# Kernel tuning notes

Measured on AMD Instinct MI355X. Metric: run time of the kernel, lower is better.

## Reference

```python
import jax, jax.numpy as jnp
import numpy as np

N_HEAD = 8
EPS = 1e-6  # LayerNorm2d eps


def setup_inputs() -> dict:
    key = jax.random.key(0)
    ks = jax.random.split(key, 7)
    B, C, H, W = 16, 256, 128, 128
    nh, dk, dv = N_HEAD, 32, 32
    s = 1.0 / np.sqrt(C)
    return {
        "q": jax.random.normal(ks[0], (B, C, H, W), jnp.float32),
        "k": jax.random.normal(ks[1], (B, C, H, W), jnp.float32),
        "v": jax.random.normal(ks[2], (B, C, H, W), jnp.float32),
        # 1x1 convs without bias == channel matmuls; weight shape [out_ch, in_ch]
        "wq": jax.random.normal(ks[3], (nh * dk, C), jnp.float32) * s,
        "wk": jax.random.normal(ks[4], (nh * dk, C), jnp.float32) * s,
        "wv": jax.random.normal(ks[5], (nh * dv, C), jnp.float32) * s,
        "wfc": jax.random.normal(ks[6], (C, nh * dv), jnp.float32) * (1.0 / np.sqrt(nh * dv)),
        "ln_w": jnp.ones((C,), jnp.float32),
        "ln_b": jnp.zeros((C,), jnp.float32),
        "kernel": 5,
        "pad": 2,
    }


def _forward(q, k, v, wq, wk, wv, wfc, ln_w, ln_b, kernel, pad):
    B, C, H, W = q.shape
    nh = N_HEAD
    dk = wq.shape[0] // nh
    dv = wv.shape[0] // nh
    assert kernel == 2 * pad + 1
    residual = q
    # 1x1 conv projections, split into heads: [B, nh, d, H, W]
    qh = jnp.einsum('oc,bchw->bohw', wq, q).reshape(B, nh, dk, H, W)
    kh = jnp.einsum('oc,bchw->bohw', wk, k).reshape(B, nh, dk, H, W)
    vh = jnp.einsum('oc,bchw->bohw', wv, v).reshape(B, nh, dv, H, W)
    # zero-pad spatially: out-of-bounds correlations/values are zero, matching the
    # original bilinear sampler (zeros padding) and the custom padding() helper.
    kp = jnp.pad(kh, ((0, 0), (0, 0), (0, 0), (pad, pad), (pad, pad)))
    vp = jnp.pad(vh, ((0, 0), (0, 0), (0, 0), (pad, pad), (pad, pad)))
    # local correlation volume: dot(q[i,j], k[i+dy-pad, j+dx-pad]) for the KxK window
    # (integer offsets -> bilinear sample degenerates to a gather). Never materializes
    # the full [B, HW, HW] matrix the torch code builds before sampling.
    corr = jnp.stack(
        [jnp.einsum('bncij,bncij->bnij', qh, kp[:, :, :, dy:dy + H, dx:dx + W])
         for dy in range(kernel) for dx in range(kernel)], axis=-1)  # [B,nh,H,W,K*K]
    # relu (from CorrBlock.corr), temperature = sqrt(d_k), softmax over window.
    # OOB entries are 0 (not -inf), faithfully matching the original.
    attn = jax.nn.softmax(jax.nn.relu(corr) / jnp.float32(np.sqrt(dk)), axis=-1)
    # channel attention: per-pixel weighted sum of v over the same window
    out = jnp.zeros((B, nh, dv, H, W), q.dtype)
    idx = 0
    for dy in range(kernel):
        for dx in range(kernel):
            out = out + attn[:, :, :, :, idx][:, :, None] * vp[:, :, :, dy:dy + H, dx:dx + W]
            idx += 1
    o = jnp.einsum('oc,bchw->bohw', wfc, out.reshape(B, nh * dv, H, W)) + residual
    # LayerNorm2d: normalize over channel dim per pixel
    mu = o.mean(1, keepdims=True)
    var = ((o - mu) ** 2).mean(1, keepdims=True)
    y = (o - mu) / jnp.sqrt(var + EPS)
    return ln_w[None, :, None, None] * y + ln_b[None, :, None, None]


def reference(q, k, v, wq, wk, wv, wfc, ln_w, ln_b, kernel, pad):
    return _forward(q, k, v, wq, wk, wv, wfc, ln_w, ln_b, kernel, pad)
```

## Files before the change

### kernel.cpp

```cpp
#include <hip/hip_runtime.h>
#include <hip/hip_bf16.h>

#define BATCH 16
#define CH 256
#define HH 128
#define WW 128
#define HWSZ (HH * WW)
#define NHEAD 8
#define DHEAD 32
#define PW 132
#define PPIX (132 * 132)
#define ROWS 264
#define ASTR 40

typedef __attribute__((ext_vector_type(8))) short bf16x8;
typedef __attribute__((ext_vector_type(4))) float f32x4;
typedef _Float16 h2v __attribute__((ext_vector_type(2)));

__device__ __forceinline__ unsigned short f2h(float f) {
    _Float16 h = (_Float16)f;
    return __builtin_bit_cast(unsigned short, h);
}
__device__ __forceinline__ unsigned pkbf(float a, float b) {
    __hip_bfloat162_raw r = __hip_bfloat162_raw(__float22bfloat162_rn(make_float2(a, b)));
    return (unsigned)r.x | ((unsigned)r.y << 16);
}
__device__ __forceinline__ int swzc(int row, int chunk) { return chunk ^ ((row >> 2) & 7); }

#if __has_builtin(__builtin_amdgcn_fdot2)
#define DOT2(a, b, c) __builtin_amdgcn_fdot2((a), (b), (c), false)
#else
#define DOT2(a, b, c) ((c) + (float)(a)[0] * (float)(b)[0] + (float)(a)[1] * (float)(b)[1])
#endif

__global__ __launch_bounds__(256)
void zpad_kernel(unsigned short* __restrict__ kpad, unsigned short* __restrict__ vpad)
{
    int bid = blockIdx.x;
    unsigned short* dst = ((bid & 1) ? vpad : kpad) + (size_t)(bid >> 1) * PPIX * DHEAD;
    const uint4 z = {0u, 0u, 0u, 0u};
    for (int i = threadIdx.x; i < 1040; i += 256) {
        int row, col;
        if (i < 264)      { row = i / 132; col = i - row * 132; }
        else if (i < 528) { int j = i - 264; int r = j / 132; row = 130 + r; col = j - r * 132; }
        else              { int j = i - 528; row = 2 + (j >> 2); int c = j & 3; col = (c < 2) ? c : (128 + c); }
        uint4* p = reinterpret_cast<uint4*>(dst + (size_t)(row * PW + col) * DHEAD);
        p[0] = z; p[1] = z; p[2] = z; p[3] = z;
    }
}

__global__ __launch_bounds__(256)
void prep_kernel(const float* __restrict__ wq, const float* __restrict__ wk,
                 const float* __restrict__ wv, const float* __restrict__ wfc,
                 unsigned short* __restrict__ wb)
{
    const float* src = (blockIdx.y == 0) ? wq : (blockIdx.y == 1) ? wk
                     : (blockIdx.y == 2) ? wv : wfc;
    unsigned short* dst = wb + blockIdx.y * 65536;
    int e = (blockIdx.x * 256 + threadIdx.x) * 8;
    const float4* s = reinterpret_cast<const float4*>(src + e);
    float4 a = s[0], c = s[1];
    uint4 u;
    u.x = pkbf(a.x, a.y); u.y = pkbf(a.z, a.w);
    u.z = pkbf(c.x, c.y); u.w = pkbf(c.z, c.w);
    *reinterpret_cast<uint4*>(dst + e) = u;
}

__global__ __launch_bounds__(512)
void proj_kernel(const float* __restrict__ q, const float* __restrict__ k,
                 const float* __restrict__ v, const unsigned short* __restrict__ wb,
                 unsigned short* __restrict__ qh, unsigned short* __restrict__ kpad,
                 unsigned short* __restrict__ vpad)
{
    __shared__ __align__(16) unsigned short lB[64 * ROWS];
    __shared__ __align__(16) unsigned short lA[2][256 * ASTR];

    const int t = threadIdx.x;
    const int b = blockIdx.y;
    const int p0 = blockIdx.x * 64;
    const int z = blockIdx.z;

    const float* X; unsigned short* Y;
    if (z == 0)      { X = q; Y = qh; }
    else if (z == 1) { X = k; Y = kpad; }
    else             { X = v; Y = vpad; }
    const unsigned short* Wb = wb + z * 65536;
    X += (size_t)b * CH * HWSZ;
    const size_t pixstride = (z == 0) ? (size_t)HWSZ : (size_t)PPIX;
    Y += (size_t)b * NHEAD * pixstride * DHEAD;

    const int lane = t & 63;
    const int wid  = t >> 6;
    const int lrow = lane & 15;
    const int lkg  = lane >> 4;
    const int pxq  = t & 15;
    const int oct  = t >> 4;
    const int ao0 = t >> 1, ak0 = (t & 1) * 2;

    {
        const float* xb = X + p0 + pxq * 4 + (size_t)(oct * 8) * HWSZ;
        float4 f0 = *reinterpret_cast<const float4*>(xb + 0 * HWSZ);
        float4 f1 = *reinterpret_cast<const float4*>(xb + 1 * HWSZ);
        float4 f2 = *reinterpret_cast<const float4*>(xb + 2 * HWSZ);
        float4 f3 = *reinterpret_cast<const float4*>(xb + 3 * HWSZ);
        float4 f4 = *reinterpret_cast<const float4*>(xb + 4 * HWSZ);
        float4 f5 = *reinterpret_cast<const float4*>(xb + 5 * HWSZ);
        float4 f6 = *reinterpret_cast<const float4*>(xb + 6 * HWSZ);
        float4 f7 = *reinterpret_cast<const float4*>(xb + 7 * HWSZ);
        uint4 u;
#define PACKJ(J, C) \
        { int row = pxq * 4 + J; \
          u.x = pkbf(f0.C, f1.C); u.y = pkbf(f2.C, f3.C); \
          u.z = pkbf(f4.C, f5.C); u.w = pkbf(f6.C, f7.C); \
          *reinterpret_cast<uint4*>(&lB[row * ROWS + swzc(row, oct) * 8]) = u; }
        PACKJ(0, x) PACKJ(1, y) PACKJ(2, z) PACKJ(3, w)
#undef PACKJ
    }
    {
        uint4 w0 = *reinterpret_cast<const uint4*>(Wb + ao0 * 256 + ak0 * 8);
        uint4 w1 = *reinterpret_cast<const uint4*>(Wb + ao0 * 256 + ak0 * 8 + 8);
        *reinterpret_cast<uint4*>(&lA[0][ao0 * ASTR + ak0 * 8]) = w0;
        *reinterpret_cast<uint4*>(&lA[0][ao0 * ASTR + ak0 * 8 + 8]) = w1;
    }

    f32x4 acc[2][4];
    const f32x4 zero = {0.f, 0.f, 0.f, 0.f};
#pragma unroll
    for (int m = 0; m < 2; ++m)
#pragma unroll
        for (int n = 0; n < 4; ++n) acc[m][n] = zero;

    __syncthreads();

#pragma unroll
    for (int ks = 0; ks < 8; ++ks) {
        uint4 w0, w1;
        if (ks < 7) {
            w0 = *reinterpret_cast<const uint4*>(Wb + ao0 * 256 + (ks + 1) * 32 + ak0 * 8);
            w1 = *reinterpret_cast<const uint4*>(Wb + ao0 * 256 + (ks + 1) * 32 + ak0 * 8 + 8);
        }
        bf16x8 af[2], bfv[4];
#pragma unroll
        for (int m = 0; m < 2; ++m)
            af[m] = *reinterpret_cast<const bf16x8*>(&lA[ks & 1][(wid * 32 + m * 16 + lrow) * ASTR + lkg * 8]);
#pragma unroll
        for (int n = 0; n < 4; ++n) {
            int row = n * 16 + lrow;
            bfv[n] = *reinterpret_cast<const bf16x8*>(&lB[row * ROWS + swzc(row, ks * 4 + lkg) * 8]);
        }
#pragma unroll
        for (int m = 0; m < 2; ++m)
#pragma unroll
            for (int n = 0; n < 4; ++n)
                acc[m][n] = __builtin_amdgcn_mfma_f32_16x16x32_bf16(af[m], bfv[n], acc[m][n], 0, 0, 0);
        if (ks < 7) {
            *reinterpret_cast<uint4*>(&lA[(ks + 1) & 1][ao0 * ASTR + ak0 * 8]) = w0;
            *reinterpret_cast<uint4*>(&lA[(ks + 1) & 1][ao0 * ASTR + ak0 * 8 + 8]) = w1;
            __syncthreads();
        }
    }

    const int lr = lane >> 4, lc = lane & 15;
#pragma unroll
    for (int m = 0; m < 2; ++m)
#pragma unroll
        for (int n = 0; n < 4; ++n) {
            int d0 = m * 16 + lr * 4;
            int p = p0 + n * 16 + lc;
            ushort4 pk;
            pk.x = f2h(acc[m][n][0]); pk.y = f2h(acc[m][n][1]);
            pk.z = f2h(acc[m][n][2]); pk.w = f2h(acc[m][n][3]);
            size_t pix;
            if (z == 0) pix = (size_t)wid * HWSZ + p;
            else { int row = p >> 7, col = p & 127; pix = (size_t)wid * PPIX + (size_t)(row + 2) * PW + (col + 2); }
            *reinterpret_cast<ushort4*>(&Y[pix * DHEAD + d0]) = pk;
        }
}

__global__ __launch_bounds__(1024)
void attn_kernel(unsigned short* __restrict__ qh,
                 const unsigned short* __restrict__ kpad,
                 const unsigned short* __restrict__ vpad)
{
    const int t = threadIdx.x;
    const int swz = (blockIdx.x & 7) * 1024 + (blockIdx.x >> 3);
    const int bh = swz >> 6;
    const int tile = swz & 63;
    const int x0 = (tile & 7) * 16, y0 = (tile >> 3) * 16;
    const int qc = t & 3;
    const int px = (t >> 2) & 15;
    const int py = t >> 6;
    const int gx = x0 + px, gy = y0 + py;

    unsigned short* qp = qh + ((size_t)bh * HWSZ + gy * WW + gx) * DHEAD + qc * 8;
    const unsigned short* kb = kpad + (size_t)bh * PPIX * DHEAD + qc * 8;
    const unsigned short* vb = vpad + (size_t)bh * PPIX * DHEAD + qc * 8;

    union { uint4 u; h2v h2[4]; } Q;
    Q.u = *reinterpret_cast<const uint4*>(qp);

    float ew[25];
#pragma unroll
    for (int wy = 0; wy < 5; ++wy) {
        const unsigned short* krow = kb + (size_t)((gy + wy) * PW + gx) * DHEAD;
#pragma unroll
        for (int wx = 0; wx < 5; ++wx) {
            union { uint4 u; h2v h2[4]; } K;
            K.u = *reinterpret_cast<const uint4*>(krow + wx * DHEAD);
            float s = 0.f;
#pragma unroll
            for (int j = 0; j < 4; ++j)
                s = DOT2(Q.h2[j], K.h2[j], s);
            s += __shfl_xor(s, 1);
            s += __shfl_xor(s, 2);
            ew[wy * 5 + wx] = __expf(fmaxf(s, 0.f) * 0.17677669529663687f);
        }
    }

    float sum = 0.f;
#pragma unroll
    for (int i = 0; i < 25; ++i) sum += ew[i];
    const float inv = 1.f / sum;

    union { uint4 u; h2v h2[4]; } A;
    const h2v hz = {(_Float16)0.f, (_Float16)0.f};
#pragma unroll
    for (int j = 0; j < 4; ++j) A.h2[j] = hz;

#pragma unroll
    for (int wy = 0; wy < 5; ++wy) {
        const unsigned short* vrow = vb + (size_t)((gy + wy) * PW + gx) * DHEAD;
#pragma unroll
        for (int wx = 0; wx < 5; ++wx) {
            _Float16 wh = (_Float16)(ew[wy * 5 + wx] * inv);
            h2v w2 = {wh, wh};
            union { uint4 u; h2v h2[4]; } V;
            V.u = *reinterpret_cast<const uint4*>(vrow + wx * DHEAD);
#pragma unroll
            for (int j = 0; j < 4; ++j)
                A.h2[j] += w2 * V.h2[j];
        }
    }

    uint4 o;
    o.x = pkbf((float)A.h2[0][0], (float)A.h2[0][1]);
    o.y = pkbf((float)A.h2[1][0], (float)A.h2[1][1]);
    o.z = pkbf((float)A.h2[2][0], (float)A.h2[2][1]);
    o.w = pkbf((float)A.h2[3][0], (float)A.h2[3][1]);
    *reinterpret_cast<uint4*>(qp) = o;
}

__global__ __launch_bounds__(512)
void fcln_kernel(const unsigned short* __restrict__ ob, const unsigned short* __restrict__ wfcb,
                 const float* __restrict__ qres, const float* __restrict__ lnw,
                 const float* __restrict__ lnb, float* __restrict__ out)
{
    __shared__ __align__(16) unsigned short lB[64 * ROWS];
    __shared__ __align__(16) unsigned short lA[2][256 * ASTR];
    __shared__ float lsum[8][64];
    __shared__ float lssq[8][64];

    const int t = threadIdx.x;
    const int b = blockIdx.y;
    const int p0 = blockIdx.x * 64;

    const int lane = t & 63;
    const int wid  = t >> 6;
    const int lrow = lane & 15;
    const int lkg  = lane >> 4;
    const int ao0 = t >> 1, ak0 = (t & 1) * 2;

#pragma unroll
    for (int r = 0; r < 4; ++r) {
        int idx = r * 512 + t;
        int h = idx >> 8;
        int rem = idx & 255;
        int px = rem >> 2, qc = rem & 3;
        uint4 bv = *reinterpret_cast<const uint4*>(
            ob + ((size_t)(b * NHEAD + h) * HWSZ + p0 + px) * DHEAD + qc * 8);
        *reinterpret_cast<uint4*>(&lB[px * ROWS + swzc(px, h * 4 + qc) * 8]) = bv;
    }
    {
        uint4 w0 = *reinterpret_cast<const uint4*>(wfcb + ao0 * 256 + ak0 * 8);
        uint4 w1 = *reinterpret_cast<const uint4*>(wfcb + ao0 * 256 + ak0 * 8 + 8);
        *reinterpret_cast<uint4*>(&lA[0][ao0 * ASTR + ak0 * 8]) = w0;
        *reinterpret_cast<uint4*>(&lA[0][ao0 * ASTR + ak0 * 8 + 8]) = w1;
    }

    f32x4 acc[2][4];
    const f32x4 zero = {0.f, 0.f, 0.f, 0.f};
#pragma unroll
    for (int m = 0; m < 2; ++m)
#pragma unroll
        for (int n = 0; n < 4; ++n) acc[m][n] = zero;

    __syncthreads();

#pragma unroll
    for (int ks = 0; ks < 8; ++ks) {
        uint4 w0, w1;
        if (ks < 7) {
            w0 = *reinterpret_cast<const uint4*>(wfcb + ao0 * 256 + (ks + 1) * 32 + ak0 * 8);
            w1 = *reinterpret_cast<const uint4*>(wfcb + ao0 * 256 + (ks + 1) * 32 + ak0 * 8 + 8);
        }
        bf16x8 af[2], bfv[4];
#pragma unroll
        for (int m = 0; m < 2; ++m)
            af[m] = *reinterpret_cast<const bf16x8*>(&lA[ks & 1][(wid * 32 + m * 16 + lrow) * ASTR + lkg * 8]);
#pragma unroll
        for (int n = 0; n < 4; ++n) {
            int row = n * 16 + lrow;
            bfv[n] = *reinterpret_cast<const bf16x8*>(&lB[row * ROWS + swzc(row, ks * 4 + lkg) * 8]);
        }
#pragma unroll
        for (int m = 0; m < 2; ++m)
#pragma unroll
            for (int n = 0; n < 4; ++n)
                acc[m][n] = __builtin_amdgcn_mfma_f32_16x16x32_bf16(af[m], bfv[n], acc[m][n], 0, 0, 0);
        if (ks < 7) {
            *reinterpret_cast<uint4*>(&lA[(ks + 1) & 1][ao0 * ASTR + ak0 * 8]) = w0;
            *reinterpret_cast<uint4*>(&lA[(ks + 1) & 1][ao0 * ASTR + ak0 * 8 + 8]) = w1;
            __syncthreads();
        }
    }

    const int lr = lane >> 4, lc = lane & 15;
    const float* qb = qres + (size_t)b * CH * HWSZ;
#pragma unroll
    for (int m = 0; m < 2; ++m)
#pragma unroll
        for (int n = 0; n < 4; ++n)
#pragma unroll
            for (int j = 0; j < 4; ++j) {
                int o = wid * 32 + m * 16 + lr * 4 + j;
                int p = p0 + n * 16 + lc;
                acc[m][n][j] += qb[(size_t)o * HWSZ + p];
            }

    float s[4], s2[4];
#pragma unroll
    for (int n = 0; n < 4; ++n) {
        float a = 0.f, c2 = 0.f;
#pragma unroll
        for (int m = 0; m < 2; ++m)
#pragma unroll
            for (int j = 0; j < 4; ++j) {
                float x = acc[m][n][j];
                a += x; c2 += x * x;
            }
        a  += __shfl_xor(a, 16);  a  += __shfl_xor(a, 32);
        c2 += __shfl_xor(c2, 16); c2 += __shfl_xor(c2, 32);
        s[n] = a; s2[n] = c2;
    }
    __syncthreads();
    if (lane < 16) {
#pragma unroll
        for (int n = 0; n < 4; ++n) {
            lsum[wid][n * 16 + lane] = s[n];
            lssq[wid][n * 16 + lane] = s2[n];
        }
    }
    __syncthreads();

    float mu[4], rs[4];
#pragma unroll
    for (int n = 0; n < 4; ++n) {
        int p = n * 16 + lc;
        float ts = 0.f, tq = 0.f;
#pragma unroll
        for (int w = 0; w < 8; ++w) { ts += lsum[w][p]; tq += lssq[w][p]; }
        float m_ = ts * (1.f / 256.f);
        float v_ = tq * (1.f / 256.f) - m_ * m_;
        mu[n] = m_;
        rs[n] = rsqrtf(v_ + 1e-6f);
    }

    float* op = out + (size_t)b * CH * HWSZ;
#pragma unroll
    for (int m = 0; m < 2; ++m)
#pragma unroll
        for (int j = 0; j < 4; ++j) {
            int o = wid * 32 + m * 16 + lr * 4 + j;
            float g = lnw[o], bb = lnb[o];
#pragma unroll
            for (int n = 0; n < 4; ++n) {
                int p = p0 + n * 16 + lc;
                op[(size_t)o * HWSZ + p] = (acc[m][n][j] - mu[n]) * rs[n] * g + bb;
            }
        }
}

extern "C" void kernel_launch(void* const* d_in, const int* in_sizes, int n_in,
                              void* d_out, int out_size, void* d_ws, size_t ws_size,
                              hipStream_t stream) {
    const float* q   = (const float*)d_in[0];
    const float* k   = (const float*)d_in[1];
    const float* v   = (const float*)d_in[2];
    const float* wq  = (const float*)d_in[3];
    const float* wk  = (const float*)d_in[4];
    const float* wv  = (const float*)d_in[5];
    const float* wfc = (const float*)d_in[6];
    const float* lnw = (const float*)d_in[7];
    const float* lnb = (const float*)d_in[8];

    const size_t qsz = (size_t)BATCH * NHEAD * HWSZ * DHEAD;
    const size_t psz = (size_t)BATCH * NHEAD * PPIX * DHEAD;
    if (ws_size < (qsz + 2 * psz + 4 * 65536) * sizeof(unsigned short)) return;

    unsigned short* qh = (unsigned short*)d_ws;
    unsigned short* kp = qh + qsz;
    unsigned short* vp = kp + psz;
    unsigned short* wb = vp + psz;

    zpad_kernel<<<256, 256, 0, stream>>>(kp, vp);
    prep_kernel<<<dim3(32, 4), 256, 0, stream>>>(wq, wk, wv, wfc, wb);
    proj_kernel<<<dim3(HWSZ / 64, BATCH, 3), 512, 0, stream>>>(q, k, v, wb, qh, kp, vp);
    attn_kernel<<<8192, 1024, 0, stream>>>(qh, kp, vp);
    fcln_kernel<<<dim3(HWSZ / 64, BATCH), 512, 0, stream>>>(qh, wb + 3 * 65536, q, lnw, lnb, (float*)d_out);
}
```

Baseline: 726.9 us.

## Make projection kernel persistent over pixel tiles with register-resident weights

The projection kernel now launches 768 blocks instead of 12288. Each block loads its weight slice once into registers as MFMA A-fragments and loops over 16 consecutive 64-pixel tiles. Activation tiles are double-buffered in LDS, with the global loads for the next tile issued ahead of the compute. This removes the repeated weight staging through LDS and the per-k-step barriers, but uses many more registers per thread and exposes fewer blocks for latency hiding.

```diff
diff --git a/kernel.cpp b/kernel.cpp
--- a/kernel.cpp
+++ b/kernel.cpp
@@ -72,13 +72,12 @@
                  unsigned short* __restrict__ qh, unsigned short* __restrict__ kpad,
                  unsigned short* __restrict__ vpad)
 {
-    __shared__ __align__(16) unsigned short lB[64 * ROWS];
-    __shared__ __align__(16) unsigned short lA[2][256 * ASTR];
+    __shared__ __align__(16) unsigned short lB[2][64 * ROWS];
 
     const int t = threadIdx.x;
-    const int b = blockIdx.y;
-    const int p0 = blockIdx.x * 64;
-    const int z = blockIdx.z;
+    const int z = blockIdx.y;
+    const int b = blockIdx.x >> 4;
+    const int pt0 = (blockIdx.x & 15) * 16;
 
     const float* X; unsigned short* Y;
     if (z == 0)      { X = q; Y = qh; }
@@ -95,86 +94,104 @@
     const int lkg  = lane >> 4;
     const int pxq  = t & 15;
     const int oct  = t >> 4;
-    const int ao0 = t >> 1, ak0 = (t & 1) * 2;
-
+
+    const float* xcol = X + (size_t)(oct * 8) * HWSZ + pxq * 4;
+
+    float4 f[8];
     {
-        const float* xb = X + p0 + pxq * 4 + (size_t)(oct * 8) * HWSZ;
-        float4 f0 = *reinterpret_cast<const float4*>(xb + 0 * HWSZ);
-        float4 f1 = *reinterpret_cast<const float4*>(xb + 1 * HWSZ);
-        float4 f2 = *reinterpret_cast<const float4*>(xb + 2 * HWSZ);
-        float4 f3 = *reinterpret_cast<const float4*>(xb + 3 * HWSZ);
-        float4 f4 = *reinterpret_cast<const float4*>(xb + 4 * HWSZ);
-        float4 f5 = *reinterpret_cast<const float4*>(xb + 5 * HWSZ);
-        float4 f6 = *reinterpret_cast<const float4*>(xb + 6 * HWSZ);
-        float4 f7 = *reinterpret_cast<const float4*>(xb + 7 * HWSZ);
-        uint4 u;
-#define PACKJ(J, C) \
-        { int row = pxq * 4 + J; \
-          u.x = pkbf(f0.C, f1.C); u.y = pkbf(f2.C, f3.C); \
-          u.z = pkbf(f4.C, f5.C); u.w = pkbf(f6.C, f7.C); \
-          *reinterpret_cast<uint4*>(&lB[row * ROWS + swzc(row, oct) * 8]) = u; }
-        PACKJ(0, x) PACKJ(1, y) PACKJ(2, z) PACKJ(3, w)
-#undef PACKJ
-    }
+        const float* xb = xcol + pt0 * 64;
+#pragma unroll
+        for (int i = 0; i < 8; ++i) f[i] = *reinterpret_cast<const float4*>(xb + (size_t)i * HWSZ);
+    }
+    bf16x8 af[2][8];
+#pragma unroll
+    for (int m = 0; m < 2; ++m)
+#pragma unroll
+        for (int ks = 0; ks < 8; ++ks)
+            af[m][ks] = *reinterpret_cast<const bf16x8*>(
+                Wb + (wid * 32 + m * 16 + lrow) * 256 + ks * 32 + lkg * 8);
+
+#define PACK_LB(BUF) do { \
+        uint4 u_; int row_; \
+        row_ = pxq * 4 + 0; \
+        u_.x = pkbf(f[0].x, f[1].x); u_.y = pkbf(f[2].x, f[3].x); \
+        u_.z = pkbf(f[4].x, f[5].x); u_.w = pkbf(f[6].x, f[7].x); \
+        *reinterpret_cast<uint4*>(&lB[BUF][row_ * ROWS + swzc(row_, oct) * 8]) = u_; \
+        row_ = pxq * 4 + 1; \
+        u_.x = pkbf(f[0].y, f[1].y); u_.y = pkbf(f[2].y, f[3].y); \
+        u_.z = pkbf(f[4].y, f[5].y); u_.w = pkbf(f[6].y, f[7].y); \
+        *reinterpret_cast<uint4*>(&lB[BUF][row_ * ROWS + swzc(row_, oct) * 8]) = u_; \
+        row_ = pxq * 4 + 2; \
+        u_.x = pkbf(f[0].z, f[1].z); u_.y = pkbf(f[2].z, f[3].z); \
+        u_.z = pkbf(f[4].z, f[5].z); u_.w = pkbf(f[6].z, f[7].z); \
+        *reinterpret_cast<uint4*>(&lB[BUF][row_ * ROWS + swzc(row_, oct) * 8]) = u_; \
+        row_ = pxq * 4 + 3; \
+        u_.x = pkbf(f[0].w, f[1].w); u_.y = pkbf(f[2].w, f[3].w); \
+        u_.z = pkbf(f[4].w, f[5].w); u_.w = pkbf(f[6].w, f[7].w); \
+        *reinterpret_cast<uint4*>(&lB[BUF][row_ * ROWS + swzc(row_, oct) * 8]) = u_; \
+    } while (0)
+
+    PACK_LB(0);
+    __syncthreads();
     {
-        uint4 w0 = *reinterpret_cast<const uint4*>(Wb + ao0 * 256 + ak0 * 8);
-        uint4 w1 = *reinterpret_cast<const uint4*>(Wb + ao0 * 256 + ak0 * 8 + 8);
-        *reinterpret_cast<uint4*>(&lA[0][ao0 * ASTR + ak0 * 8]) = w0;
-        *reinterpret_cast<uint4*>(&lA[0][ao0 * ASTR + ak0 * 8 + 8]) = w1;
-    }
-
-    f32x4 acc[2][4];
-    const f32x4 zero = {0.f, 0.f, 0.f, 0.f};
-#pragma unroll
-    for (int m = 0; m < 2; ++m)
-#pragma unroll
-        for (int n = 0; n < 4; ++n) acc[m][n] = zero;
-
-    __syncthreads();
-
-#pragma unroll
-    for (int ks = 0; ks < 8; ++ks) {
-        uint4 w0, w1;
-        if (ks < 7) {
-            w0 = *reinterpret_cast<const uint4*>(Wb + ao0 * 256 + (ks + 1) * 32 + ak0 * 8);
-            w1 = *reinterpret_cast<const uint4*>(Wb + ao0 * 256 + (ks + 1) * 32 + ak0 * 8 + 8);
-        }
-        bf16x8 af[2], bfv[4];
+        const float* xb = xcol + (pt0 + 1) * 64;
+#pragma unroll
+        for (int i = 0; i < 8; ++i) f[i] = *reinterpret_cast<const float4*>(xb + (size_t)i * HWSZ);
+    }
+
+    for (int it = 0; it < 16; ++it) {
+        f32x4 acc[2][4];
+        const f32x4 zero = {0.f, 0.f, 0.f, 0.f};
 #pragma unroll
         for (int m = 0; m < 2; ++m)
-            af[m] = *reinterpret_cast<const bf16x8*>(&lA[ks & 1][(wid * 32 + m * 16 + lrow) * ASTR + lkg * 8]);
-#pragma unroll
-        for (int n = 0; n < 4; ++n) {
-            int row = n * 16 + lrow;
-            bfv[n] = *reinterpret_cast<const bf16x8*>(&lB[row * ROWS + swzc(row, ks * 4 + lkg) * 8]);
-        }
-#pragma unroll
-        for (int m = 0; m < 2; ++m)
-#pragma unroll
-            for (int n = 0; n < 4; ++n)
-                acc[m][n] = __builtin_amdgcn_mfma_f32_16x16x32_bf16(af[m], bfv[n], acc[m][n], 0, 0, 0);
-        if (ks < 7) {
-            *reinterpret_cast<uint4*>(&lA[(ks + 1) & 1][ao0 * ASTR + ak0 * 8]) = w0;
-            *reinterpret_cast<uint4*>(&lA[(ks + 1) & 1][ao0 * ASTR + ak0 * 8 + 8]) = w1;
+#pragma unroll
+            for (int n = 0; n < 4; ++n) acc[m][n] = zero;
+
+#pragma unroll
+        for (int ks = 0; ks < 8; ++ks) {
+            bf16x8 bfv[4];
+#pragma unroll
+            for (int n = 0; n < 4; ++n) {
+                int row = n * 16 + lrow;
+                bfv[n] = *reinterpret_cast<const bf16x8*>(&lB[it & 1][row * ROWS + swzc(row, ks * 4 + lkg) * 8]);
+            }
+#pragma unroll
+            for (int m = 0; m < 2; ++m)
+#pragma unroll
+                for (int n = 0; n < 4; ++n)
+                    acc[m][n] = __builtin_amdgcn_mfma_f32_16x16x32_bf16(af[m][ks], bfv[n], acc[m][n], 0, 0, 0);
+        }
+
+        {
+            const int p0 = (pt0 + it) * 64;
+            const int lr = lane >> 4, lc = lane & 15;
+#pragma unroll
+            for (int m = 0; m < 2; ++m)
+#pragma unroll
+                for (int n = 0; n < 4; ++n) {
+                    int d0 = m * 16 + lr * 4;
+                    int p = p0 + n * 16 + lc;
+                    ushort4 pk;
+                    pk.x = f2h(acc[m][n][0]); pk.y = f2h(acc[m][n][1]);
+                    pk.z = f2h(acc[m][n][2]); pk.w = f2h(acc[m][n][3]);
+                    size_t pix;
+                    if (z == 0) pix = (size_t)wid * HWSZ + p;
+                    else { int row = p >> 7, col = p & 127; pix = (size_t)wid * PPIX + (size_t)(row + 2) * PW + (col + 2); }
+                    *reinterpret_cast<ushort4*>(&Y[pix * DHEAD + d0]) = pk;
+                }
+        }
+
+        if (it + 1 < 16) {
+            PACK_LB((it + 1) & 1);
             __syncthreads();
-        }
-    }
-
-    const int lr = lane >> 4, lc = lane & 15;
-#pragma unroll
-    for (int m = 0; m < 2; ++m)
-#pragma unroll
-        for (int n = 0; n < 4; ++n) {
-            int d0 = m * 16 + lr * 4;
-            int p = p0 + n * 16 + lc;
-            ushort4 pk;
-            pk.x = f2h(acc[m][n][0]); pk.y = f2h(acc[m][n][1]);
-            pk.z = f2h(acc[m][n][2]); pk.w = f2h(acc[m][n][3]);
-            size_t pix;
-            if (z == 0) pix = (size_t)wid * HWSZ + p;
-            else { int row = p >> 7, col = p & 127; pix = (size_t)wid * PPIX + (size_t)(row + 2) * PW + (col + 2); }
-            *reinterpret_cast<ushort4*>(&Y[pix * DHEAD + d0]) = pk;
-        }
+            if (it + 2 < 16) {
+                const float* xb = xcol + (pt0 + it + 2) * 64;
+#pragma unroll
+                for (int i = 0; i < 8; ++i) f[i] = *reinterpret_cast<const float4*>(xb + (size_t)i * HWSZ);
+            }
+        }
+    }
+#undef PACK_LB
 }
 
 __global__ __launch_bounds__(1024)
@@ -414,7 +431,7 @@
 
     zpad_kernel<<<256, 256, 0, stream>>>(kp, vp);
     prep_kernel<<<dim3(32, 4), 256, 0, stream>>>(wq, wk, wv, wfc, wb);
-    proj_kernel<<<dim3(HWSZ / 64, BATCH, 3), 512, 0, stream>>>(q, k, v, wb, qh, kp, vp);
+    proj_kernel<<<dim3(256, 3), 512, 0, stream>>>(q, k, v, wb, qh, kp, vp);
     attn_kernel<<<8192, 1024, 0, stream>>>(qh, kp, vp);
     fcln_kernel<<<dim3(HWSZ / 64, BATCH), 512, 0, stream>>>(qh, wb + 3 * 65536, q, lnw, lnb, (float*)d_out);
 }
```

Measured after the change: 690.7 us. -5.0%, faster.
